# Kernel tuning notes

Measured on AMD Instinct MI355X. Metric: run time of the kernel, lower is better.

## Reference

```python
import jax, jax.numpy as jnp
import numpy as np

N = 50000      # nodes
E = 800000     # edges (before self-loops)
F_IN = 256     # nfeat
HEADS = 8      # nhead
C1 = 16        # hidden_sizes (per-head channels of conv1)
NCLS = 40      # nclass
NEG_SLOPE = 0.2


def setup_inputs() -> dict:
    key = jax.random.key(0)
    ks = jax.random.split(key, 12)
    s = 0.1
    x = jax.random.normal(ks[0], (N, F_IN), dtype=jnp.float32)
    edge_index = jax.random.randint(ks[1], (2, E), 0, N, dtype=jnp.int64)
    edge_attr = jax.random.normal(ks[2], (E,), dtype=jnp.float32)  # unused by forward
    W1 = jax.random.normal(ks[3], (F_IN, HEADS * C1), dtype=jnp.float32) * s
    att_src1 = jax.random.normal(ks[4], (HEADS, C1), dtype=jnp.float32) * s
    att_dst1 = jax.random.normal(ks[5], (HEADS, C1), dtype=jnp.float32) * s
    b1 = jnp.zeros((HEADS * C1,), dtype=jnp.float32)
    W2 = jax.random.normal(ks[6], (HEADS * C1, NCLS), dtype=jnp.float32) * s
    att_src2 = jax.random.normal(ks[7], (1, NCLS), dtype=jnp.float32) * s
    att_dst2 = jax.random.normal(ks[8], (1, NCLS), dtype=jnp.float32) * s
    b2 = jnp.zeros((NCLS,), dtype=jnp.float32)
    return {"x": x, "edge_index": edge_index, "edge_attr": edge_attr,
            "W1": W1, "att_src1": att_src1, "att_dst1": att_dst1, "b1": b1,
            "W2": W2, "att_src2": att_src2, "att_dst2": att_dst2, "b2": b2}


def gat_layer(x, W, att_src, att_dst, bias, src, dst, concat):
    """PyG-style GATConv (eval mode, no dropout). src/dst include self-loops."""
    H, C = att_src.shape
    h = (x @ W).reshape(-1, H, C)                     # [N,H,C]
    a_src = (h * att_src[None]).sum(-1)               # [N,H]
    a_dst = (h * att_dst[None]).sum(-1)               # [N,H]
    e = jax.nn.leaky_relu(a_src[src] + a_dst[dst], NEG_SLOPE)  # [Etot,H]
    # segment softmax over destination neighborhoods
    m = jax.ops.segment_max(e, dst, num_segments=N)   # [N,H]
    m = jax.lax.stop_gradient(jnp.where(jnp.isfinite(m), m, 0.0))
    p = jnp.exp(e - m[dst])
    denom = jax.ops.segment_sum(p, dst, num_segments=N)
    alpha = p / (denom[dst] + 1e-16)                  # [Etot,H]
    out = jax.ops.segment_sum(alpha[:, :, None] * h[src], dst, num_segments=N)  # [N,H,C]
    out = out.reshape(-1, H * C) if concat else out.mean(axis=1)
    return out + bias


def reference(x, edge_index, edge_attr, W1, att_src1, att_dst1, b1, W2, att_src2, att_dst2, b2):
    # add self loops (PyG GATConv default)
    loops = jnp.arange(N, dtype=edge_index.dtype)
    src = jnp.concatenate([edge_index[0], loops])
    dst = jnp.concatenate([edge_index[1], loops])
    # eval mode: F.dropout is identity
    h = jax.nn.elu(gat_layer(x, W1, att_src1, att_dst1, b1, src, dst, concat=True))
    final = gat_layer(h, W2, att_src2, att_dst2, b2, src, dst, concat=False)
    return final, jax.nn.log_softmax(final, axis=1)
```

## Files before the change

kernel.cpp:

```cpp
#include <hip/hip_runtime.h>

#define NN 50000
#define EE 800000
#define FIN 256
#define HD 8
#define C1 16
#define HC 128
#define NC 40
#define NEG 0.2f
#define CAP 64
#define R2 32
#define BM 64
#define GB1 ((NN + BM - 1) / BM)
#define NP_N (NN / 8)
#define SCB 2048

typedef __attribute__((ext_vector_type(8))) short short8;
typedef __attribute__((ext_vector_type(4))) float f32x4;
union FragU { uint4 u; short8 s; };

__device__ __forceinline__ float leaky(float v){ return v > 0.f ? v : NEG * v; }

__device__ __forceinline__ unsigned int f2bf(float f){
  unsigned int u = __float_as_uint(f);
  u += 0x7fffu + ((u >> 16) & 1u);
  return u >> 16;
}
__device__ __forceinline__ unsigned int pack2bf(float a, float b){
  return f2bf(a) | (f2bf(b) << 16);
}
__device__ __forceinline__ float bflo(unsigned int u){ return __uint_as_float(u << 16); }
__device__ __forceinline__ float bfhi(unsigned int u){ return __uint_as_float(u & 0xffff0000u); }
__device__ __forceinline__ float bfus(unsigned short u){ return __uint_as_float((unsigned int)u << 16); }

__global__ __launch_bounds__(256) void k_prep(const float* __restrict__ W1,
                                              uint4* __restrict__ W1bfs,
                                              const int* __restrict__ ei,
                                              int* __restrict__ cnt,
                                              int* __restrict__ srcp){
  const int tid = threadIdx.x;
  if (blockIdx.x < 16){
    int f = blockIdx.x * 256 + tid;
    int lane = f & 63, nt = (f >> 6) & 7, kt = f >> 9;
    int quad = lane >> 4, l16 = lane & 15;
    const float* src = W1 + (size_t)(kt * 32 + quad * 8) * HC + nt * 16 + l16;
    unsigned int p[4];
#pragma unroll
    for (int jj = 0; jj < 4; jj++){
      float v0 = src[(size_t)(2 * jj) * HC];
      float v1 = src[(size_t)(2 * jj + 1) * HC];
      p[jj] = pack2bf(v0, v1);
    }
    W1bfs[f] = make_uint4(p[0], p[1], p[2], p[3]);
    return;
  }
  const int b = blockIdx.x - 16;
  const int part = b & 7, rank = b >> 3;
  const int lo = part * NP_N, hi = lo + NP_N;
  for (int e = rank * 256 + tid; e < EE; e += 256 * 256){
    int d = ei[EE + e];
    if (d >= lo && d < hi){
      int s = ei[e];
      int pos = atomicAdd(&cnt[d], 1);
      if (pos < CAP) srcp[d * CAP + pos] = s;
    }
  }
}

__global__ __launch_bounds__(256, 3) void k_gemm1(const float* __restrict__ x,
                                                  const uint4* __restrict__ W1bfs,
                                                  const float* __restrict__ att_s,
                                                  const float* __restrict__ att_d,
                                                  unsigned short* __restrict__ h1b,
                                                  float* __restrict__ as1,
                                                  float* __restrict__ ad1){
  const int tid = threadIdx.x;
  const int wave = tid >> 6, lane = tid & 63;
  const int quad = lane >> 4, l16 = lane & 15;
  const int m0 = blockIdx.x * BM + wave * 16;
  int arow = m0 + l16; if (arow >= NN) arow = NN - 1;
  const float* xr = x + (size_t)arow * FIN;

  float4 xa[16];
#pragma unroll
  for (int kt = 0; kt < 8; kt++){
    xa[2 * kt]     = *(const float4*)(xr + kt * 32 + quad * 8);
    xa[2 * kt + 1] = *(const float4*)(xr + kt * 32 + quad * 8 + 4);
  }
  FragU bf[8];
#pragma unroll
  for (int nt = 0; nt < 8; nt++) bf[nt].u = W1bfs[nt * 64 + lane];

  f32x4 acc[8];
#pragma unroll
  for (int t = 0; t < 8; t++) acc[t] = (f32x4){0.f, 0.f, 0.f, 0.f};

#pragma unroll
  for (int kt = 0; kt < 8; kt++){
    FragU bn[8];
    if (kt < 7){
#pragma unroll
      for (int nt = 0; nt < 8; nt++)
        bn[nt].u = W1bfs[((kt + 1) * 8 + nt) * 64 + lane];
    }
    FragU af;
    af.u = make_uint4(pack2bf(xa[2 * kt].x,     xa[2 * kt].y),
                      pack2bf(xa[2 * kt].z,     xa[2 * kt].w),
                      pack2bf(xa[2 * kt + 1].x, xa[2 * kt + 1].y),
                      pack2bf(xa[2 * kt + 1].z, xa[2 * kt + 1].w));
#pragma unroll
    for (int nt = 0; nt < 8; nt++)
      acc[nt] = __builtin_amdgcn_mfma_f32_16x16x32_bf16(af.s, bf[nt].s, acc[nt], 0, 0, 0);
    if (kt < 7){
#pragma unroll
      for (int nt = 0; nt < 8; nt++) bf[nt] = bn[nt];
    }
  }

  float sv[8], dv[8];
#pragma unroll
  for (int h = 0; h < 8; h++){ sv[h] = att_s[h * 16 + l16]; dv[h] = att_d[h * 16 + l16]; }
#pragma unroll
  for (int r = 0; r < 4; r++){
    const int gr = m0 + quad * 4 + r;
    float s[8], d[8];
#pragma unroll
    for (int h = 0; h < 8; h++){ s[h] = acc[h][r] * sv[h]; d[h] = acc[h][r] * dv[h]; }
#pragma unroll
    for (int o = 1; o < 16; o <<= 1){
#pragma unroll
      for (int h = 0; h < 8; h++){ s[h] += __shfl_xor(s[h], o); d[h] += __shfl_xor(d[h], o); }
    }
    if (gr < NN){
#pragma unroll
      for (int h = 0; h < 8; h++)
        h1b[(size_t)gr * HC + h * 16 + l16] = (unsigned short)f2bf(acc[h][r]);
      if (l16 == 0){
        *(float4*)(as1 + gr * 8)     = make_float4(s[0], s[1], s[2], s[3]);
        *(float4*)(as1 + gr * 8 + 4) = make_float4(s[4], s[5], s[6], s[7]);
        *(float4*)(ad1 + gr * 8)     = make_float4(d[0], d[1], d[2], d[3]);
        *(float4*)(ad1 + gr * 8 + 4) = make_float4(d[4], d[5], d[6], d[7]);
      }
    }
  }
}

__global__ __launch_bounds__(256) void k_agg1(const int* __restrict__ srcp,
                                              const int* __restrict__ cnt,
                                              const float* __restrict__ as1,
                                              const float* __restrict__ ad1,
                                              const unsigned short* __restrict__ h1b,
                                              const float* __restrict__ b1,
                                              unsigned short* __restrict__ h2b){
  __shared__ float wls[4][64][8];
  __shared__ int   sls[4][64];
  const int lane = threadIdx.x & 63, w = threadIdx.x >> 6;
  const int n = blockIdx.x * 4 + w;
  int deg = cnt[n]; if (deg > CAP - 1) deg = CAP - 1;
  const int nE = deg + 1;
  int sA = n;
  if (lane < deg) sA = srcp[n * CAP + lane];
  sls[w][lane] = sA;

  const int h = lane >> 3, e8 = lane & 7;
  const float adg = ad1[n * 8 + h];
  int nCh = (nE + 7) >> 3; if (nCh < 2) nCh = 2;

  float mx = -3.0e38f;
  for (int c = 0; c < nCh; c++){
    const int i = c * 8 + e8;
    const int s = sls[w][i];
    const float v = (i < nE) ? leaky(as1[(size_t)s * 8 + h] + adg) : -3.0e38f;
    wls[w][i][h] = v;
    mx = fmaxf(mx, v);
  }
  mx = fmaxf(mx, __shfl_xor(mx, 1));
  mx = fmaxf(mx, __shfl_xor(mx, 2));
  mx = fmaxf(mx, __shfl_xor(mx, 4));

  float den = 0.f;
  for (int c = 0; c < nCh; c++){
    const int i = c * 8 + e8;
    const float v = wls[w][i][h];
    const float wt = (i < nE) ? __expf(v - mx) : 0.f;
    wls[w][i][h] = wt;
    den += wt;
  }
  den += __shfl_xor(den, 1);
  den += __shfl_xor(den, 2);
  den += __shfl_xor(den, 4);

  const unsigned int* hp = (const unsigned int*)h1b;
  float ax = 0.f, ay = 0.f;
  {
    unsigned int u[16]; float q[16];
#pragma unroll
    for (int i = 0; i < 16; i++){
      u[i] = hp[(size_t)(unsigned)((sls[w][i] << 6) + lane)];
      q[i] = wls[w][i][h];
    }
#pragma unroll
    for (int i = 0; i < 16; i++){ ax += q[i] * bflo(u[i]); ay += q[i] * bfhi(u[i]); }
  }
  for (int i0 = 16; i0 < nE; i0 += 8){
    unsigned int uu[8]; float qq[8];
#pragma unroll
    for (int t = 0; t < 8; t++){
      const int j = i0 + t, p = min(j, deg);
      uu[t] = hp[(size_t)(unsigned)((sls[w][p] << 6) + lane)];
      qq[t] = (j < nE) ? wls[w][p][h] : 0.f;
    }
#pragma unroll
    for (int t = 0; t < 8; t++){ ax += qq[t] * bflo(uu[t]); ay += qq[t] * bfhi(uu[t]); }
  }

  const float invd = 1.f / (den + 1e-16f);
  const float2 bb = *(const float2*)(b1 + 2 * lane);
  float ox = ax * invd + bb.x;
  float oy = ay * invd + bb.y;
  ox = ox > 0.f ? ox : (__expf(ox) - 1.f);
  oy = oy > 0.f ? oy : (__expf(oy) - 1.f);
  *(unsigned int*)(h2b + (size_t)n * HC + 2 * lane) = pack2bf(ox, oy);
}

__global__ __launch_bounds__(256) void k_gemm2(const unsigned short* __restrict__ h2b,
                                               const float* __restrict__ W2,
                                               const float* __restrict__ att_s2,
                                               const float* __restrict__ att_d2,
                                               unsigned short* __restrict__ gb,
                                               float* __restrict__ as2,
                                               float* __restrict__ ad2){
  __shared__ float hs[R2][HC + 2];
  __shared__ float w2s[HC * NC];
  const int tid = threadIdx.x;
  const int r0 = blockIdx.x * R2;
  for (int i = tid; i < HC * NC; i += 256) w2s[i] = W2[i];
  for (int i = tid; i < R2 * (HC / 2); i += 256){
    int r = i / (HC / 2), c = i % (HC / 2);
    unsigned int u = (r0 + r < NN) ? ((const unsigned int*)h2b)[(size_t)(r0 + r) * (HC / 2) + c] : 0u;
    hs[r][2 * c]     = bflo(u);
    hs[r][2 * c + 1] = bfhi(u);
  }
  __syncthreads();
  const int r = tid >> 3, j = tid & 7;
  float acc[5] = {0.f, 0.f, 0.f, 0.f, 0.f};
  for (int k = 0; k < HC; k++){
    float hv = hs[r][k];
#pragma unroll
    for (int q = 0; q < 5; q++) acc[q] += hv * w2s[k * NC + j + 8 * q];
  }
  const int node = r0 + r;
  if (node < NN){
    float s = 0.f, d = 0.f;
#pragma unroll
    for (int q = 0; q < 5; q++){
      int c = j + 8 * q;
      gb[(size_t)node * NC + c] = (unsigned short)f2bf(acc[q]);
      s += acc[q] * att_s2[c];
      d += acc[q] * att_d2[c];
    }
#pragma unroll
    for (int o = 1; o < 8; o <<= 1){ s += __shfl_xor(s, o); d += __shfl_xor(d, o); }
    if (j == 0){ as2[node] = s; ad2[node] = d; }
  }
}

__global__ __launch_bounds__(256) void k_agg2(const int* __restrict__ srcp,
                                              const int* __restrict__ cnt,
                                              const float* __restrict__ as2,
                                              const float* __restrict__ ad2,
                                              const unsigned short* __restrict__ gb,
                                              const float* __restrict__ b2,
                                              float* __restrict__ out){
  __shared__ float wls[4][64];
  __shared__ int   sls[4][64];
  const int lane = threadIdx.x & 63, w = threadIdx.x >> 6;
  const int n = blockIdx.x * 4 + w;
  int deg = cnt[n]; if (deg > CAP - 1) deg = CAP - 1;
  const int nE = deg + 1;
  const bool act = (lane <= deg);
  int sA = n;
  if (lane < deg) sA = srcp[n * CAP + lane];
  sls[w][lane] = sA;
  const float ad = ad2[n];
  float v = act ? leaky(as2[sA] + ad) : -3.0e38f;
  float mx = v;
#pragma unroll
  for (int o = 1; o < 64; o <<= 1) mx = fmaxf(mx, __shfl_xor(mx, o));
  float wt = act ? __expf(v - mx) : 0.f;
  float den = wt;
#pragma unroll
  for (int o = 1; o < 64; o <<= 1) den += __shfl_xor(den, o);
  wls[w][lane] = wt;

  const int c = min(lane, NC - 1);
  float acc = 0.f;
  {
    float g[16], q[16];
#pragma unroll
    for (int i = 0; i < 16; i++){
      g[i] = bfus(gb[(size_t)(unsigned)(sls[w][i] * NC + c)]);
      q[i] = wls[w][i];
    }
#pragma unroll
    for (int i = 0; i < 16; i++) acc += q[i] * g[i];
  }
  for (int i0 = 16; i0 < nE; i0 += 8){
    float gg[8], qq[8];
#pragma unroll
    for (int t = 0; t < 8; t++){
      const int j = i0 + t;
      gg[t] = bfus(gb[(size_t)(unsigned)(sls[w][j] * NC + c)]);
      qq[t] = wls[w][j];
    }
#pragma unroll
    for (int t = 0; t < 8; t++) acc += qq[t] * gg[t];
  }
  const float invd = 1.f / (den + 1e-16f);
  const bool cl = (lane < NC);
  float f = acc * invd + b2[c];
  if (cl) out[(size_t)n * NC + lane] = f;
  float fv = cl ? f : -3.4e38f;
  float m2 = fv;
#pragma unroll
  for (int o = 1; o < 64; o <<= 1) m2 = fmaxf(m2, __shfl_xor(m2, o));
  float ex = cl ? __expf(fv - m2) : 0.f;
#pragma unroll
  for (int o = 1; o < 64; o <<= 1) ex += __shfl_xor(ex, o);
  const float lse = m2 + __logf(ex);
  if (cl) out[(size_t)(NN * NC) + (size_t)n * NC + lane] = fv - lse;
}

extern "C" void kernel_launch(void* const* d_in, const int* in_sizes, int n_in,
                              void* d_out, int out_size, void* d_ws, size_t ws_size,
                              hipStream_t stream){
  const float* x      = (const float*)d_in[0];
  const int*   ei     = (const int*)  d_in[1];
  const float* W1     = (const float*)d_in[3];
  const float* att_s1 = (const float*)d_in[4];
  const float* att_d1 = (const float*)d_in[5];
  const float* b1     = (const float*)d_in[6];
  const float* W2     = (const float*)d_in[7];
  const float* att_s2 = (const float*)d_in[8];
  const float* att_d2 = (const float*)d_in[9];
  const float* b2     = (const float*)d_in[10];
  float* out = (float*)d_out;

  char* wp = (char*)d_ws;
  uint4* W1bfs = (uint4*)wp;                 wp += (size_t)4096 * 16;
  unsigned short* h1b = (unsigned short*)wp; wp += (size_t)NN * HC * 2;
  unsigned short* h2b = (unsigned short*)wp; wp += (size_t)NN * HC * 2;
  unsigned short* gb  = (unsigned short*)wp; wp += (size_t)NN * NC * 2;
  float* as1 = (float*)wp;                   wp += (size_t)NN * HD * 4;
  float* ad1 = (float*)wp;                   wp += (size_t)NN * HD * 4;
  float* as2 = (float*)wp;                   wp += (size_t)NN * 4;
  float* ad2 = (float*)wp;                   wp += (size_t)NN * 4;
  int* cnt   = (int*)wp;                     wp += (size_t)NN * 4;
  int* srcp  = (int*)wp;                     wp += (size_t)NN * CAP * 4;

  hipMemsetAsync(cnt, 0, (size_t)NN * sizeof(int), stream);
  k_prep  <<<16 + SCB, 256, 0, stream>>>(W1, W1bfs, ei, cnt, srcp);
  k_gemm1 <<<GB1, 256, 0, stream>>>(x, W1bfs, att_s1, att_d1, h1b, as1, ad1);
  k_agg1  <<<NN / 4, 256, 0, stream>>>(srcp, cnt, as1, ad1, h1b, b1, h2b);
  k_gemm2 <<<(NN + R2 - 1) / R2, 256, 0, stream>>>(h2b, W2, att_s2, att_d2, gb, as2, ad2);
  k_agg2  <<<NN / 4, 256, 0, stream>>>(srcp, cnt, as2, ad2, gb, b2, out);
}
```

Baseline: 259.8 us.

## Fold edge bucketing into GEMM1 launch and widen aggregation blocks

The edge-to-destination bucketing (atomic scatter into srcp) moves out of the prep kernel and into extra trailing blocks of the layer-1 GEMM launch. The memory-bound scatter can then overlap with the compute-bound GEMM instead of running serially ahead of it. Both aggregation kernels now use 512-thread blocks handling 8 nodes each, and store pre-scaled source offsets in shared memory so the gather loops skip per-element multiplies and the min() clamp. The risk is that the scatter blocks compete with GEMM blocks for occupancy, and the larger blocks change scheduling granularity.

```diff
diff --git a/kernel.cpp b/kernel.cpp
--- a/kernel.cpp
+++ b/kernel.cpp
@@ -34,47 +34,45 @@
 __device__ __forceinline__ float bfus(unsigned short u){ return __uint_as_float((unsigned int)u << 16); }
 
 __global__ __launch_bounds__(256) void k_prep(const float* __restrict__ W1,
-                                              uint4* __restrict__ W1bfs,
-                                              const int* __restrict__ ei,
-                                              int* __restrict__ cnt,
-                                              int* __restrict__ srcp){
-  const int tid = threadIdx.x;
-  if (blockIdx.x < 16){
-    int f = blockIdx.x * 256 + tid;
-    int lane = f & 63, nt = (f >> 6) & 7, kt = f >> 9;
-    int quad = lane >> 4, l16 = lane & 15;
-    const float* src = W1 + (size_t)(kt * 32 + quad * 8) * HC + nt * 16 + l16;
-    unsigned int p[4];
-#pragma unroll
-    for (int jj = 0; jj < 4; jj++){
-      float v0 = src[(size_t)(2 * jj) * HC];
-      float v1 = src[(size_t)(2 * jj + 1) * HC];
-      p[jj] = pack2bf(v0, v1);
-    }
-    W1bfs[f] = make_uint4(p[0], p[1], p[2], p[3]);
-    return;
-  }
-  const int b = blockIdx.x - 16;
-  const int part = b & 7, rank = b >> 3;
-  const int lo = part * NP_N, hi = lo + NP_N;
-  for (int e = rank * 256 + tid; e < EE; e += 256 * 256){
-    int d = ei[EE + e];
-    if (d >= lo && d < hi){
-      int s = ei[e];
-      int pos = atomicAdd(&cnt[d], 1);
-      if (pos < CAP) srcp[d * CAP + pos] = s;
-    }
-  }
+                                              uint4* __restrict__ W1bfs){
+  int f = blockIdx.x * 256 + threadIdx.x;
+  int lane = f & 63, nt = (f >> 6) & 7, kt = f >> 9;
+  int quad = lane >> 4, l16 = lane & 15;
+  const float* src = W1 + (size_t)(kt * 32 + quad * 8) * HC + nt * 16 + l16;
+  unsigned int p[4];
+#pragma unroll
+  for (int jj = 0; jj < 4; jj++){
+    float v0 = src[(size_t)(2 * jj) * HC];
+    float v1 = src[(size_t)(2 * jj + 1) * HC];
+    p[jj] = pack2bf(v0, v1);
+  }
+  W1bfs[f] = make_uint4(p[0], p[1], p[2], p[3]);
 }
 
 __global__ __launch_bounds__(256, 3) void k_gemm1(const float* __restrict__ x,
                                                   const uint4* __restrict__ W1bfs,
                                                   const float* __restrict__ att_s,
                                                   const float* __restrict__ att_d,
+                                                  const int* __restrict__ ei,
                                                   unsigned short* __restrict__ h1b,
                                                   float* __restrict__ as1,
-                                                  float* __restrict__ ad1){
+                                                  float* __restrict__ ad1,
+                                                  int* __restrict__ cnt,
+                                                  int* __restrict__ srcp){
   const int tid = threadIdx.x;
+  if (blockIdx.x >= GB1){
+    const int part = blockIdx.x & 7, rank = (blockIdx.x - GB1) >> 3;
+    const int lo = part * NP_N, hi = lo + NP_N;
+    for (int e = rank * 256 + tid; e < EE; e += 256 * 256){
+      int d = ei[EE + e];
+      if (d >= lo && d < hi){
+        int s = ei[e];
+        int pos = atomicAdd(&cnt[d], 1);
+        if (pos < CAP) srcp[d * CAP + pos] = s;
+      }
+    }
+    return;
+  }
   const int wave = tid >> 6, lane = tid & 63;
   const int quad = lane >> 4, l16 = lane & 15;
   const int m0 = blockIdx.x * BM + wave * 16;
@@ -145,22 +143,22 @@
   }
 }
 
-__global__ __launch_bounds__(256) void k_agg1(const int* __restrict__ srcp,
+__global__ __launch_bounds__(512) void k_agg1(const int* __restrict__ srcp,
                                               const int* __restrict__ cnt,
                                               const float* __restrict__ as1,
                                               const float* __restrict__ ad1,
                                               const unsigned short* __restrict__ h1b,
                                               const float* __restrict__ b1,
                                               unsigned short* __restrict__ h2b){
-  __shared__ float wls[4][64][8];
-  __shared__ int   sls[4][64];
+  __shared__ float wls[8][64][8];
+  __shared__ int   sls[8][64];
   const int lane = threadIdx.x & 63, w = threadIdx.x >> 6;
-  const int n = blockIdx.x * 4 + w;
+  const int n = blockIdx.x * 8 + w;
   int deg = cnt[n]; if (deg > CAP - 1) deg = CAP - 1;
   const int nE = deg + 1;
   int sA = n;
   if (lane < deg) sA = srcp[n * CAP + lane];
-  sls[w][lane] = sA;
+  sls[w][lane] = sA << 6;
 
   const int h = lane >> 3, e8 = lane & 7;
   const float adg = ad1[n * 8 + h];
@@ -169,8 +167,8 @@
   float mx = -3.0e38f;
   for (int c = 0; c < nCh; c++){
     const int i = c * 8 + e8;
-    const int s = sls[w][i];
-    const float v = (i < nE) ? leaky(as1[(size_t)s * 8 + h] + adg) : -3.0e38f;
+    const int s8 = sls[w][i] >> 3;
+    const float v = (i < nE) ? leaky(as1[(size_t)(unsigned)(s8 + h)] + adg) : -3.0e38f;
     wls[w][i][h] = v;
     mx = fmaxf(mx, v);
   }
@@ -196,7 +194,7 @@
     unsigned int u[16]; float q[16];
 #pragma unroll
     for (int i = 0; i < 16; i++){
-      u[i] = hp[(size_t)(unsigned)((sls[w][i] << 6) + lane)];
+      u[i] = hp[(size_t)(unsigned)(sls[w][i] + lane)];
       q[i] = wls[w][i][h];
     }
 #pragma unroll
@@ -206,9 +204,9 @@
     unsigned int uu[8]; float qq[8];
 #pragma unroll
     for (int t = 0; t < 8; t++){
-      const int j = i0 + t, p = min(j, deg);
-      uu[t] = hp[(size_t)(unsigned)((sls[w][p] << 6) + lane)];
-      qq[t] = (j < nE) ? wls[w][p][h] : 0.f;
+      const int j = i0 + t;
+      uu[t] = hp[(size_t)(unsigned)(sls[w][j] + lane)];
+      qq[t] = (j < nE) ? wls[w][j][h] : 0.f;
     }
 #pragma unroll
     for (int t = 0; t < 8; t++){ ax += qq[t] * bflo(uu[t]); ay += qq[t] * bfhi(uu[t]); }
@@ -265,25 +263,25 @@
   }
 }
 
-__global__ __launch_bounds__(256) void k_agg2(const int* __restrict__ srcp,
+__global__ __launch_bounds__(512) void k_agg2(const int* __restrict__ srcp,
                                               const int* __restrict__ cnt,
                                               const float* __restrict__ as2,
                                               const float* __restrict__ ad2,
                                               const unsigned short* __restrict__ gb,
                                               const float* __restrict__ b2,
                                               float* __restrict__ out){
-  __shared__ float wls[4][64];
-  __shared__ int   sls[4][64];
+  __shared__ float wls[8][64];
+  __shared__ int   sls[8][64];
   const int lane = threadIdx.x & 63, w = threadIdx.x >> 6;
-  const int n = blockIdx.x * 4 + w;
+  const int n = blockIdx.x * 8 + w;
   int deg = cnt[n]; if (deg > CAP - 1) deg = CAP - 1;
   const int nE = deg + 1;
   const bool act = (lane <= deg);
   int sA = n;
   if (lane < deg) sA = srcp[n * CAP + lane];
-  sls[w][lane] = sA;
   const float ad = ad2[n];
   float v = act ? leaky(as2[sA] + ad) : -3.0e38f;
+  sls[w][lane] = sA * NC;
   float mx = v;
 #pragma unroll
   for (int o = 1; o < 64; o <<= 1) mx = fmaxf(mx, __shfl_xor(mx, o));
@@ -299,7 +297,7 @@
     float g[16], q[16];
 #pragma unroll
     for (int i = 0; i < 16; i++){
-      g[i] = bfus(gb[(size_t)(unsigned)(sls[w][i] * NC + c)]);
+      g[i] = bfus(gb[(size_t)(unsigned)(sls[w][i] + c)]);
       q[i] = wls[w][i];
     }
 #pragma unroll
@@ -310,7 +308,7 @@
 #pragma unroll
     for (int t = 0; t < 8; t++){
       const int j = i0 + t;
-      gg[t] = bfus(gb[(size_t)(unsigned)(sls[w][j] * NC + c)]);
+      gg[t] = bfus(gb[(size_t)(unsigned)(sls[w][j] + c)]);
       qq[t] = wls[w][j];
     }
 #pragma unroll
@@ -359,9 +357,9 @@
   int* srcp  = (int*)wp;                     wp += (size_t)NN * CAP * 4;
 
   hipMemsetAsync(cnt, 0, (size_t)NN * sizeof(int), stream);
-  k_prep  <<<16 + SCB, 256, 0, stream>>>(W1, W1bfs, ei, cnt, srcp);
-  k_gemm1 <<<GB1, 256, 0, stream>>>(x, W1bfs, att_s1, att_d1, h1b, as1, ad1);
-  k_agg1  <<<NN / 4, 256, 0, stream>>>(srcp, cnt, as1, ad1, h1b, b1, h2b);
+  k_prep  <<<16, 256, 0, stream>>>(W1, W1bfs);
+  k_gemm1 <<<GB1 + SCB, 256, 0, stream>>>(x, W1bfs, att_s1, att_d1, ei, h1b, as1, ad1, cnt, srcp);
+  k_agg1  <<<NN / 8, 512, 0, stream>>>(srcp, cnt, as1, ad1, h1b, b1, h2b);
   k_gemm2 <<<(NN + R2 - 1) / R2, 256, 0, stream>>>(h2b, W2, att_s2, att_d2, gb, as2, ad2);
-  k_agg2  <<<NN / 4, 256, 0, stream>>>(srcp, cnt, as2, ad2, gb, b2, out);
-}
+  k_agg2  <<<NN / 8, 512, 0, stream>>>(srcp, cnt, as2, ad2, gb, b2, out);
+}
```

After: 254.4 us. 1.02x faster.
